# Performance work log

Hardware: AMD Instinct MI355X
Metric: run time of the kernel (lower is better)

The kernel has to match this reference:

```python
import jax, jax.numpy as jnp
import numpy as np

B, S, E, H = 4, 2048, 1024, 16
D = E // H  # head_dim = 64
ROPE_BASE = 10000.0


def _rope(x):
    # x: [B, H, S, D] -> rotary position embedding applied over seq dim
    seq_len = x.shape[2]
    inv_freq = 1.0 / (ROPE_BASE ** (jnp.arange(0, D, 2, dtype=jnp.float32) / D))  # [D/2]
    freqs = jnp.arange(seq_len, dtype=jnp.float32)[:, None] * inv_freq[None, :]   # [S, D/2]
    emb = jnp.concatenate([freqs, freqs], axis=-1)                                 # [S, D]
    cos = jnp.cos(emb).astype(x.dtype)
    sin = jnp.sin(emb).astype(x.dtype)
    x1, x2 = jnp.split(x, 2, axis=-1)
    rotated = jnp.concatenate([-x2, x1], axis=-1)
    return x * cos + rotated * sin


def setup_inputs() -> dict:
    key = jax.random.key(0)
    ks = jax.random.split(key, 10)
    p = 0.02
    return {
        "x": jax.random.normal(ks[0], (B, S, E), dtype=jnp.float32),
        "Wq": jax.random.normal(ks[1], (E, E), dtype=jnp.float32) * p,
        "bq": jnp.zeros((E,), dtype=jnp.float32),
        "Wk": jax.random.normal(ks[2], (E, E), dtype=jnp.float32) * p,
        "bk": jnp.zeros((E,), dtype=jnp.float32),
        "Wv": jax.random.normal(ks[3], (E, E), dtype=jnp.float32) * p,
        "bv": jnp.zeros((E,), dtype=jnp.float32),
        "Wo": jax.random.normal(ks[4], (E, E), dtype=jnp.float32) * p,
        "bo": jnp.zeros((E,), dtype=jnp.float32),
        "key_padding_mask": jnp.zeros((B, S), dtype=bool),
    }


def reference(x, Wq, bq, Wk, bk, Wv, bv, Wo, bo, key_padding_mask):
    b, s, _ = x.shape
    # QKV projections -> [B, H, S, D]
    def proj(W, bias):
        return (x @ W + bias).reshape(b, s, H, D).transpose(0, 2, 1, 3)
    q = _rope(proj(Wq, bq))
    k = _rope(proj(Wk, bk))
    v = proj(Wv, bv)
    scale = D ** -0.5
    scores = jnp.einsum('bhqd,bhkd->bhqk', q, k) * scale  # [B, H, S, S]
    scores = jnp.where(key_padding_mask[:, None, None, :], jnp.finfo(scores.dtype).min, scores)
    probs = jax.nn.softmax(scores, axis=-1)
    out = jnp.einsum('bhqk,bhkd->bhqd', probs, v)         # [B, H, S, D]
    out = out.transpose(0, 2, 1, 3).reshape(b, s, E)
    return out @ Wo + bo
```

## Files before the change

kernel.cpp:

```cpp
#include <hip/hip_runtime.h>
#include <hip/hip_bf16.h>
#include <math.h>

#define Bn 4
#define Sn 2048
#define En 1024
#define Hn 16
#define Dn 64
#define Mn (Bn * Sn)

typedef __attribute__((ext_vector_type(8))) short short8;
typedef __attribute__((ext_vector_type(4))) short short4v;
typedef __attribute__((ext_vector_type(4))) float f32x4;
typedef __attribute__((ext_vector_type(16))) float f32x16;
typedef __attribute__((ext_vector_type(2))) unsigned int uint2v;

#if __has_builtin(__builtin_amdgcn_exp2f)
#define EXP2(x) __builtin_amdgcn_exp2f(x)
#else
#define EXP2(x) exp2f(x)
#endif

#if __has_builtin(__builtin_amdgcn_permlane32_swap)
#define HAVE_PLSWAP 1
#endif

#define GLOAD16(g, s) __builtin_amdgcn_global_load_lds( \
    (const __attribute__((address_space(1))) unsigned int*)(g), \
    (__attribute__((address_space(3))) unsigned int*)(s), 16, 0, 0)

__device__ inline unsigned short f2bf(float f) {
    unsigned int u = __float_as_uint(f);
    u += 0x7FFFu + ((u >> 16) & 1u);
    return (unsigned short)(u >> 16);
}
__device__ inline float bf2f(unsigned short h) {
    return __uint_as_float(((unsigned int)h) << 16);
}
__device__ inline void split2(float f, unsigned short& hi, unsigned short& lo) {
    hi = f2bf(f);
    lo = f2bf(f - bf2f(hi));
}
__device__ inline short8 ld8s(const unsigned short* p) {
    union { short4v h[2]; short8 v; } r;
    r.h[0] = *(const short4v*)p;
    r.h[1] = *(const short4v*)(p + 4);
    return r.v;
}
__device__ inline short8 g8(const unsigned short* p) {
    union { int4 i; short8 v; } r;
    r.i = *(const int4*)p;
    return r.v;
}

__device__ inline void st16(unsigned short* base, int row, int col16, int4 v) {
    const unsigned off = ((unsigned)(row * 128 + col16 * 2)) ^ ((unsigned)((row & 7) << 4));
    *(int4*)((char*)base + off) = v;
}
__device__ inline short8 ld16(const unsigned short* base, int row, int col16) {
    const unsigned off = ((unsigned)(row * 128 + col16 * 2)) ^ ((unsigned)((row & 7) << 4));
    union { int4 i; short8 v; } r;
    r.i = *(const int4*)((const char*)base + off);
    return r.v;
}

__global__ void rope_table_kernel(float* __restrict__ ct, float* __restrict__ st) {
    int i = blockIdx.x * blockDim.x + threadIdx.x;
    if (i < Sn * 32) {
        int s = i >> 5, p = i & 31;
        double inv = pow(10000.0, -(double)p / 32.0);
        double a = (double)s * inv;
        ct[i] = (float)cos(a);
        st[i] = (float)sin(a);
    }
}

__global__ __launch_bounds__(256) void convx_kernel(
    const float* __restrict__ X, unsigned short* __restrict__ Xh) {
    int i = blockIdx.x * 256 + threadIdx.x;
    float4 v = ((const float4*)X)[i];
    float f[4] = {v.x, v.y, v.z, v.w};
    short4v h;
#pragma unroll
    for (int j = 0; j < 4; ++j) h[j] = (short)f2bf(f[j]);
    ((short4v*)Xh)[i] = h;
}

__global__ __launch_bounds__(256) void tconv4_kernel(
    const float* __restrict__ Wq, const float* __restrict__ Wk,
    const float* __restrict__ Wv, const float* __restrict__ Wo,
    unsigned short* __restrict__ WqkvT, unsigned short* __restrict__ WoT2) {
    const int m = blockIdx.z;
    const float* W = (m == 0) ? Wq : (m == 1) ? Wk : (m == 2) ? Wv : Wo;
    unsigned short* dst = (m < 3) ? WqkvT + (size_t)m * En * En : WoT2;
    const int rowLen = (m < 3) ? En : 2048;
    const int dup = (m == 3);

    __shared__ float Ws[64][65];
    const int t = threadIdx.x;
    const int kb = blockIdx.y * 64, nb = blockIdx.x * 64;
    const int lr = t >> 2, lc = (t & 3) * 16;
#pragma unroll
    for (int u = 0; u < 4; ++u) {
        float4 v = *(const float4*)&W[(size_t)(kb + lr) * En + nb + lc + 4 * u];
        Ws[lr][lc + 4 * u + 0] = v.x; Ws[lr][lc + 4 * u + 1] = v.y;
        Ws[lr][lc + 4 * u + 2] = v.z; Ws[lr][lc + 4 * u + 3] = v.w;
    }
    __syncthreads();
    const int orow = t >> 2, ock = (t & 3) * 16;
#pragma unroll
    for (int u = 0; u < 4; ++u) {
        short4v hs;
#pragma unroll
        for (int j = 0; j < 4; ++j) hs[j] = (short)f2bf(Ws[ock + 4 * u + j][orow]);
        unsigned short* dp = &dst[(size_t)(nb + orow) * rowLen + kb + ock + 4 * u];
        *(short4v*)dp = hs;
        if (dup) *(short4v*)(dp + 1024) = hs;
    }
}

__global__ __launch_bounds__(256) void vtrans_kernel(
    const unsigned short* __restrict__ Vb, unsigned short* __restrict__ VbT) {
    __shared__ unsigned short Ts[64][68];
    const int t = threadIdx.x;
    const int bh = blockIdx.y;
    const int s0 = blockIdx.x * 64;
    const size_t ibase = (size_t)bh * Sn * Dn;
    const int lr = t >> 2, lc = (t & 3) * 16;
    int4 i0 = *(const int4*)&Vb[ibase + (size_t)(s0 + lr) * Dn + lc];
    int4 i1 = *(const int4*)&Vb[ibase + (size_t)(s0 + lr) * Dn + lc + 8];
    *(int2*)&Ts[lr][lc] = make_int2(i0.x, i0.y);
    *(int2*)&Ts[lr][lc + 4] = make_int2(i0.z, i0.w);
    *(int2*)&Ts[lr][lc + 8] = make_int2(i1.x, i1.y);
    *(int2*)&Ts[lr][lc + 12] = make_int2(i1.z, i1.w);
    __syncthreads();
    const int dr = t >> 2, sc = (t & 3) * 16;
    unsigned short o[16];
#pragma unroll
    for (int j = 0; j < 16; ++j) o[j] = Ts[sc + j][dr];
    unsigned short* op = &VbT[(size_t)bh * Dn * Sn + (size_t)dr * Sn + s0 + sc];
    *(int4*)&op[0] = *(int4*)&o[0];
    *(int4*)&op[8] = *(int4*)&o[8];
}

template <int KN, int EPI>
__global__ __launch_bounds__(256) void gemm97(
    const unsigned short* __restrict__ A, const unsigned short* __restrict__ Bt,
    const float* __restrict__ b0, const float* __restrict__ bkv,
    const float* __restrict__ bvv,
    unsigned short* __restrict__ oQ, unsigned short* __restrict__ oK,
    unsigned short* __restrict__ oV, float* __restrict__ oF,
    const float* __restrict__ ct, const float* __restrict__ st) {
    __shared__ unsigned short As[128][64];
    __shared__ unsigned short Bs[128][64];
    const int t = threadIdx.x;
    const int w = t >> 6, l = t & 63;
    const int wm = w & 1, wn = w >> 1;
    const int q = l >> 4, ln16 = l & 15;
    const int r8 = l >> 3, i8 = l & 7;
    const int m0 = blockIdx.y * 128, n0 = blockIdx.x * 128;

    f32x4 acc[4][4];
#pragma unroll
    for (int i = 0; i < 4; ++i)
#pragma unroll
        for (int j = 0; j < 4; ++j)
#pragma unroll
            for (int r = 0; r < 4; ++r) acc[i][j][r] = 0.0f;

    const unsigned short* Ag = &A[(size_t)(m0 + 32 * w + r8) * KN + 8 * i8];
    const unsigned short* Bg = &Bt[(size_t)(n0 + 32 * w + r8) * KN + 8 * i8];

    for (int k0 = 0; k0 < KN; k0 += 64) {
        __syncthreads();
#pragma unroll
        for (int j = 0; j < 4; ++j) {
            GLOAD16(Ag + (size_t)(8 * j) * KN + k0, &As[32 * w + 8 * j][0]);
            GLOAD16(Bg + (size_t)(8 * j) * KN + k0, &Bs[32 * w + 8 * j][0]);
        }
        __syncthreads();
#pragma unroll
        for (int ks = 0; ks < 2; ++ks) {
            short8 af[4], bf[4];
#pragma unroll
            for (int i = 0; i < 4; ++i)
                af[i] = ld8s(&As[64 * wm + 16 * i + ln16][32 * ks + 8 * q]);
#pragma unroll
            for (int j = 0; j < 4; ++j)
                bf[j] = ld8s(&Bs[64 * wn + 16 * j + ln16][32 * ks + 8 * q]);
#pragma unroll
            for (int i = 0; i < 4; ++i)
#pragma unroll
                for (int j = 0; j < 4; ++j)
                    acc[i][j] = __builtin_amdgcn_mfma_f32_16x16x32_bf16(
                        af[i], bf[j], acc[i][j], 0, 0, 0);
        }
    }

    if (EPI == 0) {
#pragma unroll
        for (int i = 0; i < 4; ++i)
#pragma unroll
            for (int r = 0; r < 4; ++r) {
                const int m = m0 + 64 * wm + 16 * i + 4 * q + r;
#pragma unroll
                for (int j = 0; j < 4; ++j) {
                    const int n = n0 + 64 * wn + 16 * j + ln16;
                    oF[(size_t)m * En + n] = acc[i][j][r] + b0[n];
                }
            }
    } else {
        const int mat = n0 >> 10;
        const int nIn = (n0 & 1023) + 64 * wn;
        const int hh = nIn >> 6;
        const float* bias = (mat == 0) ? b0 : (mat == 1) ? bkv : bvv;
        unsigned short* op = (mat == 0) ? oQ : (mat == 1) ? oK : oV;
#pragma unroll
        for (int i = 0; i < 4; ++i)
#pragma unroll
            for (int r = 0; r < 4; ++r) {
                const int m = m0 + 64 * wm + 16 * i + 4 * q + r;
                const int b = m >> 11, s2 = m & (Sn - 1);
                const size_t base = (((size_t)(b * Hn + hh)) * Sn + s2) * Dn;
#pragma unroll
                for (int j = 0; j < 2; ++j) {
                    const int nh = 16 * j + ln16;
                    float v0 = acc[i][j][r] + bias[nIn + nh];
                    float v1 = acc[i][j + 2][r] + bias[nIn + nh + 32];
                    if (mat <= 1) {
                        float c = ct[s2 * 32 + nh], sn = st[s2 * 32 + nh];
                        float o0 = v0 * c - v1 * sn;
                        float o1 = v1 * c + v0 * sn;
                        if (mat == 0) {
                            o0 *= 0.18033688011112042f;
                            o1 *= 0.18033688011112042f;
                        }
                        v0 = o0; v1 = o1;
                    }
                    op[base + nh] = f2bf(v0);
                    op[base + nh + 32] = f2bf(v1);
                }
            }
    }
}

__global__ __launch_bounds__(256) void attn_mfma_kernel(
    const unsigned short* __restrict__ Qb, const unsigned short* __restrict__ Kb,
    const unsigned short* __restrict__ VbT, const unsigned char* __restrict__ mask,
    unsigned short* __restrict__ Obuf) {
    __shared__ __align__(16) unsigned short Ks[2][64][64];
    __shared__ __align__(16) unsigned short Vs[2][64][64];

    const int t = threadIdx.x;
    const int w = t >> 6, l = t & 63, h2 = l >> 5, ln = l & 31;
    const int q0 = blockIdx.x * 128;
    const int h = blockIdx.y, b = blockIdx.z;
    const size_t ho = ((size_t)(b * Hn + h)) * Sn * Dn;
    const unsigned char* maskB = mask + (size_t)b * Sn;

    short8 qh[4];
    const int qrow = q0 + 32 * w + ln;
#pragma unroll
    for (int s = 0; s < 4; ++s)
        qh[s] = g8(&Qb[ho + (size_t)qrow * Dn + 16 * s + 8 * h2]);

    f32x16 accO0, accO1;
#pragma unroll
    for (int i = 0; i < 16; ++i) { accO0[i] = 0.0f; accO1[i] = 0.0f; }
    float lsum[4] = {0.0f, 0.0f, 0.0f, 0.0f};

    const int kr = t >> 2, kc = (t & 3) * 16;
    const unsigned short* Kp = &Kb[ho + (size_t)kr * Dn + kc];
    const unsigned short* Vp = &VbT[ho + (size_t)kr * Sn + kc];

    int4 ck0 = *(const int4*)Kp, ck1 = *(const int4*)(Kp + 8);
    int4 cv0 = *(const int4*)Vp, cv1 = *(const int4*)(Vp + 8);
    unsigned char cm = maskB[l];

#pragma unroll 2
    for (int kt = 0; kt < Sn / 64; ++kt) {
        const int pb = kt & 1;
        unsigned short* KsP = &Ks[pb][0][0];
        unsigned short* VsP = &Vs[pb][0][0];
        st16(KsP, kr, kc, ck0); st16(KsP, kr, kc + 8, ck1);
        st16(VsP, kr, kc, cv0); st16(VsP, kr, kc + 8, cv1);
        const unsigned long long bm = __ballot(cm != 0);
        __syncthreads();
        const int kn = ((kt + 1) & (Sn / 64 - 1)) * 64;
        ck0 = *(const int4*)(Kp + (size_t)kn * Dn);
        ck1 = *(const int4*)(Kp + (size_t)kn * Dn + 8);
        cv0 = *(const int4*)(Vp + kn);
        cv1 = *(const int4*)(Vp + kn + 8);
        cm = maskB[kn + l];

#pragma unroll
        for (int c = 0; c < 2; ++c) {
            short8 kf[4];
#pragma unroll
            for (int s = 0; s < 4; ++s)
                kf[s] = ld16(KsP, 32 * c + ln, 16 * s + 8 * h2);
            f32x16 accS;
#pragma unroll
            for (int i = 0; i < 16; ++i) accS[i] = 0.0f;
            __builtin_amdgcn_s_setprio(1);
#pragma unroll
            for (int s = 0; s < 4; ++s)
                accS = __builtin_amdgcn_mfma_f32_32x32x16_bf16(kf[s], qh[s], accS, 0, 0, 0);
            __builtin_amdgcn_s_setprio(0);

            unsigned pw[8];
#pragma unroll
            for (int g = 0; g < 4; ++g)
#pragma unroll
                for (int j = 0; j < 2; ++j) {
                    const int r0 = 4 * g + 2 * j;
                    float p0 = EXP2(accS[r0]);
                    float p1 = EXP2(accS[r0 + 1]);
                    if (bm) {
                        const int key = 32 * c + 8 * g + 4 * h2 + 2 * j;
                        if ((bm >> key) & 1) p0 = 0.0f;
                        if ((bm >> (key + 1)) & 1) p1 = 0.0f;
                    }
                    const unsigned u0 = __float_as_uint(p0) & 0xFFFF0000u;
                    const unsigned u1 = __float_as_uint(p1) & 0xFFFF0000u;
                    lsum[g] += __uint_as_float(u0);
                    lsum[g] += __uint_as_float(u1);
                    pw[2 * g + j] = (u0 >> 16) | u1;
                }

#pragma unroll
            for (int s = 0; s < 2; ++s) {
                union { unsigned u[4]; short8 v; } af;
#ifdef HAVE_PLSWAP
                uint2v r02 = __builtin_amdgcn_permlane32_swap(
                    pw[4 * s + 0], pw[4 * s + 2], false, false);
                uint2v r13 = __builtin_amdgcn_permlane32_swap(
                    pw[4 * s + 1], pw[4 * s + 3], false, false);
                af.u[0] = r02[0]; af.u[1] = r13[0];
                af.u[2] = r02[1]; af.u[3] = r13[1];
#else
                const unsigned x0 = pw[4 * s + 0], x1 = pw[4 * s + 1];
                const unsigned y0 = pw[4 * s + 2], y1 = pw[4 * s + 3];
                const unsigned py0 = (unsigned)__shfl_xor((int)y0, 32);
                const unsigned py1 = (unsigned)__shfl_xor((int)y1, 32);
                const unsigned px0 = (unsigned)__shfl_xor((int)x0, 32);
                const unsigned px1 = (unsigned)__shfl_xor((int)x1, 32);
                af.u[0] = h2 ? py0 : x0;
                af.u[1] = h2 ? py1 : x1;
                af.u[2] = h2 ? y0 : px0;
                af.u[3] = h2 ? y1 : px1;
#endif
                short8 vA = ld16(VsP, ln, 32 * c + 16 * s + 8 * h2);
                short8 vB = ld16(VsP, 32 + ln, 32 * c + 16 * s + 8 * h2);
                __builtin_amdgcn_s_setprio(1);
                accO0 = __builtin_amdgcn_mfma_f32_32x32x16_bf16(af.v, vA, accO0, 0, 0, 0);
                accO1 = __builtin_amdgcn_mfma_f32_32x32x16_bf16(af.v, vB, accO1, 0, 0, 0);
                __builtin_amdgcn_s_setprio(0);
            }
        }
    }

    const float lme = (lsum[0] + lsum[1]) + (lsum[2] + lsum[3]);
    const float tot = lme + __shfl_xor(lme, 32);
    const float linv = 1.0f / fmaxf(tot, 1e-37f);
#pragma unroll
    for (int r = 0; r < 16; ++r) {
        const int row = (r & 3) + 8 * (r >> 2) + 4 * h2;
        const float lr = __shfl(linv, row);
        const int s = q0 + 32 * w + row;
        const size_t base = ((size_t)b * Sn + s) * 2048 + h * Dn;
        unsigned short a, b2;
        split2(accO0[r] * lr, a, b2);
        Obuf[base + ln] = a; Obuf[base + 1024 + ln] = b2;
        split2(accO1[r] * lr, a, b2);
        Obuf[base + 32 + ln] = a; Obuf[base + 1024 + 32 + ln] = b2;
    }
}

extern "C" void kernel_launch(void* const* d_in, const int* in_sizes, int n_in,
                              void* d_out, int out_size, void* d_ws, size_t ws_size,
                              hipStream_t stream) {
    const float* x  = (const float*)d_in[0];
    const float* Wq = (const float*)d_in[1];
    const float* bq = (const float*)d_in[2];
    const float* Wk = (const float*)d_in[3];
    const float* bk = (const float*)d_in[4];
    const float* Wv = (const float*)d_in[5];
    const float* bv = (const float*)d_in[6];
    const float* Wo = (const float*)d_in[7];
    const float* bo = (const float*)d_in[8];
    const unsigned char* mask = (const unsigned char*)d_in[9];

    const size_t NE = (size_t)Mn * En;
    const size_t WN = (size_t)En * En;
    unsigned short* ws = (unsigned short*)d_ws;
    unsigned short* Xh = ws;
    unsigned short* Qb = Xh + NE;
    unsigned short* Kb = Qb + NE;
    unsigned short* Vb = Kb + NE;
    unsigned short* VbT = Vb + NE;
    unsigned short* Obuf = VbT + NE;
    unsigned short* WqkvT = Obuf + 2 * NE;
    unsigned short* WoT2 = WqkvT + 3 * WN;
    float* ct = (float*)(WoT2 + 2 * WN);
    float* st = ct + (size_t)Sn * 32;

    rope_table_kernel<<<(Sn * 32 + 255) / 256, 256, 0, stream>>>(ct, st);
    convx_kernel<<<(int)(NE / 1024), 256, 0, stream>>>(x, Xh);
    tconv4_kernel<<<dim3(16, 16, 4), 256, 0, stream>>>(
        Wq, Wk, Wv, Wo, WqkvT, WoT2);

    gemm97<En, 1><<<dim3(3 * En / 128, Mn / 128), 256, 0, stream>>>(
        Xh, WqkvT, bq, bk, bv, Qb, Kb, Vb, nullptr, ct, st);

    vtrans_kernel<<<dim3(Sn / 64, Bn * Hn), 256, 0, stream>>>(Vb, VbT);

    attn_mfma_kernel<<<dim3(Sn / 128, Hn, Bn), 256, 0, stream>>>(
        Qb, Kb, VbT, mask, Obuf);

    gemm97<2048, 0><<<dim3(En / 128, Mn / 128), 256, 0, stream>>>(
        Obuf, WoT2, bo, nullptr, nullptr, nullptr, nullptr, nullptr,
        (float*)d_out, ct, st);
}
```

Baseline: 342.2 us.

## Fold RoPE table into weight conversion, remap GEMM blocks, round softmax probs

```diff
diff --git a/kernel.cpp b/kernel.cpp
--- a/kernel.cpp
+++ b/kernel.cpp
@@ -64,17 +64,6 @@
     return r.v;
 }
 
-__global__ void rope_table_kernel(float* __restrict__ ct, float* __restrict__ st) {
-    int i = blockIdx.x * blockDim.x + threadIdx.x;
-    if (i < Sn * 32) {
-        int s = i >> 5, p = i & 31;
-        double inv = pow(10000.0, -(double)p / 32.0);
-        double a = (double)s * inv;
-        ct[i] = (float)cos(a);
-        st[i] = (float)sin(a);
-    }
-}
-
 __global__ __launch_bounds__(256) void convx_kernel(
     const float* __restrict__ X, unsigned short* __restrict__ Xh) {
     int i = blockIdx.x * 256 + threadIdx.x;
@@ -86,11 +75,21 @@
     ((short4v*)Xh)[i] = h;
 }
 
-__global__ __launch_bounds__(256) void tconv4_kernel(
+__global__ __launch_bounds__(256) void tconv5_kernel(
     const float* __restrict__ Wq, const float* __restrict__ Wk,
     const float* __restrict__ Wv, const float* __restrict__ Wo,
-    unsigned short* __restrict__ WqkvT, unsigned short* __restrict__ WoT2) {
+    unsigned short* __restrict__ WqkvT, unsigned short* __restrict__ WoT2,
+    float* __restrict__ ct, float* __restrict__ st) {
     const int m = blockIdx.z;
+    if (m == 4) {
+        const int i = (blockIdx.y * 16 + blockIdx.x) * 256 + threadIdx.x;
+        const int s = i >> 5, p = i & 31;
+        double inv = pow(10000.0, -(double)p / 32.0);
+        double a = (double)s * inv;
+        ct[i] = (float)cos(a);
+        st[i] = (float)sin(a);
+        return;
+    }
     const float* W = (m == 0) ? Wq : (m == 1) ? Wk : (m == 2) ? Wv : Wo;
     unsigned short* dst = (m < 3) ? WqkvT + (size_t)m * En * En : WoT2;
     const int rowLen = (m < 3) ? En : 2048;
@@ -158,7 +157,18 @@
     const int wm = w & 1, wn = w >> 1;
     const int q = l >> 4, ln16 = l & 15;
     const int r8 = l >> 3, i8 = l & 7;
-    const int m0 = blockIdx.y * 128, n0 = blockIdx.x * 128;
+
+    int bx = blockIdx.x, by = blockIdx.y;
+    {
+        const int gx = gridDim.x;
+        const int nwg = gx * gridDim.y;
+        if ((nwg & 7) == 0) {
+            const int n = by * gx + bx;
+            const int s = (n & 7) * (nwg >> 3) + (n >> 3);
+            bx = s % gx; by = s / gx;
+        }
+    }
+    const int m0 = by * 128, n0 = bx * 128;
 
     f32x4 acc[4][4];
 #pragma unroll
@@ -321,11 +331,10 @@
                         if ((bm >> key) & 1) p0 = 0.0f;
                         if ((bm >> (key + 1)) & 1) p1 = 0.0f;
                     }
-                    const unsigned u0 = __float_as_uint(p0) & 0xFFFF0000u;
-                    const unsigned u1 = __float_as_uint(p1) & 0xFFFF0000u;
-                    lsum[g] += __uint_as_float(u0);
-                    lsum[g] += __uint_as_float(u1);
-                    pw[2 * g + j] = (u0 >> 16) | u1;
+                    lsum[g] += p0 + p1;
+                    union { __hip_bfloat162 h; unsigned u; } cv;
+                    cv.h = __float22bfloat162_rn(make_float2(p0, p1));
+                    pw[2 * g + j] = cv.u;
                 }
 
 #pragma unroll
@@ -405,10 +414,9 @@
     float* ct = (float*)(WoT2 + 2 * WN);
     float* st = ct + (size_t)Sn * 32;
 
-    rope_table_kernel<<<(Sn * 32 + 255) / 256, 256, 0, stream>>>(ct, st);
     convx_kernel<<<(int)(NE / 1024), 256, 0, stream>>>(x, Xh);
-    tconv4_kernel<<<dim3(16, 16, 4), 256, 0, stream>>>(
-        Wq, Wk, Wv, Wo, WqkvT, WoT2);
+    tconv5_kernel<<<dim3(16, 16, 5), 256, 0, stream>>>(
+        Wq, Wk, Wv, Wo, WqkvT, WoT2, ct, st);
 
     gemm97<En, 1><<<dim3(3 * En / 128, Mn / 128), 256, 0, stream>>>(
         Xh, WqkvT, bq, bk, bv, Qb, Kb, Vb, nullptr, ct, st);
```

After: 346.1 us. About the same (+1.1%).
